# Kernel optimization log

Hardware: AMD Instinct MI355X
Metric: run time of the kernel (lower is better)

The kernel has to match this reference:

```python
import jax, jax.numpy as jnp
import numpy as np

TEMPERATURE = 0.07
NEG = -1e30  # safe stand-in for -inf (keeps grads NaN-free)


def setup_inputs() -> dict:
    key = jax.random.key(0)
    k1, k2 = jax.random.split(key)
    semantic_state = jax.random.normal(k1, (8, 1024, 64), dtype=jnp.float32)
    token_ids = jax.random.randint(k2, (8, 1024), 0, 1000)
    return {"semantic_state": semantic_state, "token_ids": token_ids}


def reference(semantic_state, token_ids):
    # semantic_state: [B, T, D], token_ids: [B, T]
    B, T, D = semantic_state.shape
    N = B * T
    x = semantic_state.reshape(N, D)
    tok = token_ids.reshape(N)

    # L2 normalize (F.normalize, eps=1e-12)
    nrm = jnp.sqrt(jnp.sum(x * x, axis=1, keepdims=True))
    z = x / jnp.maximum(nrm, 1e-12)

    # full cosine-similarity matrix [N, N]
    S = z @ z.T

    # pairs: same token id, excluding self (the per-group similarity structure)
    same = tok[:, None] == tok[None, :]
    eye = jnp.eye(N, dtype=bool)
    mask = same & ~eye

    # per-anchor contrastive term: -logsumexp_{j != i, tok_j == tok_i}(-S_ij / T)
    logits = jnp.where(mask, -S / TEMPERATURE, NEG)
    lse = jax.nn.logsumexp(logits, axis=1)

    valid = mask.any(axis=1)  # anchors whose token repeats (count >= 2)
    per_anchor = jnp.where(valid, -lse, 0.0)

    num_pairs = jnp.sum(mask)  # == sum over groups of N_g*(N_g-1)
    loss = jnp.where(
        num_pairs > 0,
        jnp.sum(per_anchor) / jnp.maximum(num_pairs, 1).astype(S.dtype),
        jnp.array(0.0, dtype=S.dtype),
    )
    return loss
```

## Files before the change

kernel.cpp:

```cpp
#include <hip/hip_runtime.h>
#include <math.h>

#define TEMP 0.07f
#define NTOK 1024
#define CAP 64

__global__ __launch_bounds__(256) void prep_kernel(const float* __restrict__ x,
        const int* __restrict__ tok, float* __restrict__ invn,
        int* __restrict__ cursor, int* __restrict__ bucket, int n) {
    const int lane = threadIdx.x & 63;
    const int w = blockIdx.x * 4 + (threadIdx.x >> 6);
    const int sub = lane & 7, mem = lane >> 3;
    const int row = w * 8 + mem;
    if (row >= n) return;
    const float4* xr = (const float4*)&x[row * 64 + sub * 8];
    float4 a = xr[0], b = xr[1];
    float s = a.x * a.x + a.y * a.y + a.z * a.z + a.w * a.w
            + b.x * b.x + b.y * b.y + b.z * b.z + b.w * b.w;
    s += __shfl_xor(s, 1, 64);
    s += __shfl_xor(s, 2, 64);
    s += __shfl_xor(s, 4, 64);
    if (sub == 0) {
        invn[row] = 1.0f / fmaxf(sqrtf(s), 1e-12f);
        int g = tok[row];
        int slot = atomicAdd(&cursor[g], 1);
        if (slot < CAP) bucket[g * CAP + slot] = row;
    }
}

__global__ __launch_bounds__(256) void lse_kernel(const float* __restrict__ x,
        const int* __restrict__ tok, const float* __restrict__ invn,
        const int* __restrict__ cursor, const int* __restrict__ bucket,
        float* __restrict__ per_anchor, int n) {
    const int lane = threadIdx.x & 63;
    const int i = blockIdx.x * 4 + (threadIdx.x >> 6);
    if (i >= n) return;
    const int g = tok[i];
    const int cnt = min(cursor[g], CAP);
    if (cnt < 2) {
        if (lane == 0) per_anchor[i] = 0.0f;
        return;
    }
    const int sub = lane & 7, mem = lane >> 3;
    const float4* zr = (const float4*)&x[i * 64 + sub * 8];
    float4 za = zr[0], zb = zr[1];
    float sc = invn[i] * (1.0f / TEMP);
    za.x *= sc; za.y *= sc; za.z *= sc; za.w *= sc;
    zb.x *= sc; zb.y *= sc; zb.z *= sc; zb.w *= sc;
    const int* bk = &bucket[g * CAP];
    float S = 0.0f;
    for (int m0 = 0; m0 < cnt; m0 += 8) {
        int mm = m0 + mem;
        bool act = (mm < cnt);
        int j = act ? bk[mm] : 0;
        act = act && (j != i);
        const float4* xr = (const float4*)&x[j * 64 + sub * 8];
        float4 a = xr[0], b = xr[1];
        float iv = invn[j];
        float d = za.x * a.x + za.y * a.y + za.z * a.z + za.w * a.w
                + zb.x * b.x + zb.y * b.y + zb.z * b.z + zb.w * b.w;
        d += __shfl_xor(d, 1, 64);
        d += __shfl_xor(d, 2, 64);
        d += __shfl_xor(d, 4, 64);
        float e = act ? __expf(-d * iv) : 0.0f;
        S += (sub == 0) ? e : 0.0f;
    }
    S += __shfl_xor(S, 8, 64);
    S += __shfl_xor(S, 16, 64);
    S += __shfl_xor(S, 32, 64);
    if (lane == 0) per_anchor[i] = -__logf(S);
}

__global__ __launch_bounds__(1024) void finalize_kernel(
        const float* __restrict__ per_anchor, const int* __restrict__ cursor,
        float* __restrict__ out, int n) {
    int t = threadIdx.x;
    double s = 0.0;
    const float4* pa4 = (const float4*)per_anchor;
    int n4 = n >> 2;
    for (int k = t; k < n4; k += 1024) {
        float4 v = pa4[k];
        s += (double)v.x + (double)v.y + (double)v.z + (double)v.w;
    }
    for (int k = (n4 << 2) + t; k < n; k += 1024) s += (double)per_anchor[k];
    long long c = cursor[t];
    long long p = c * (c - 1);
    #pragma unroll
    for (int o = 32; o; o >>= 1) {
        s += __shfl_xor(s, o, 64);
        p += __shfl_xor(p, o, 64);
    }
    __shared__ double    ls[16];
    __shared__ long long lp[16];
    int wid = t >> 6, lane = t & 63;
    if (lane == 0) { ls[wid] = s; lp[wid] = p; }
    __syncthreads();
    if (wid == 0) {
        double fs = (lane < 16) ? ls[lane] : 0.0;
        long long fp = (lane < 16) ? lp[lane] : 0;
        #pragma unroll
        for (int o = 8; o; o >>= 1) {
            fs += __shfl_xor(fs, o, 64);
            fp += __shfl_xor(fp, o, 64);
        }
        if (lane == 0) out[0] = (fp > 0) ? (float)(fs / (double)fp) : 0.0f;
    }
}

extern "C" void kernel_launch(void* const* d_in, const int* in_sizes, int n_in,
                              void* d_out, int out_size, void* d_ws, size_t ws_size,
                              hipStream_t stream) {
    const float* x = (const float*)d_in[0];
    const int* tok = (const int*)d_in[1];
    int n = in_sizes[1];

    char* ws = (char*)d_ws;
    size_t o = 0;
    int* cursor = (int*)(ws + o);         o += NTOK * 4;
    float* invn = (float*)(ws + o);       o += ((size_t)n * 4 + 255) & ~255UL;
    int* bucket = (int*)(ws + o);         o += (size_t)NTOK * CAP * 4;
    float* per_anchor = (float*)(ws + o);

    hipMemsetAsync(cursor, 0, NTOK * 4, stream);
    prep_kernel<<<(n + 31) / 32, 256, 0, stream>>>(x, tok, invn, cursor, bucket, n);
    lse_kernel<<<(n + 3) / 4, 256, 0, stream>>>(x, tok, invn, cursor, bucket,
                                                per_anchor, n);
    finalize_kernel<<<1, NTOK, 0, stream>>>(per_anchor, cursor, (float*)d_out, n);
}
```

Before: 21.71 us.

## Bucket tokens with shared-memory atomics in one block and recompute norms inline

Replaces the memset plus multi-block prep kernel with a single 1024-thread block that counts and buckets token ids using LDS atomics, then writes the cursors out. Row norms are no longer precomputed into a workspace array; the LSE kernel recomputes each anchor's and each partner's squared norm alongside the dot product, sharing the same shuffle reduction. This drops one launch and the memset, and removes the invn buffer and its global atomics. In exchange, all bucketing is serialized onto one CU and each pair does extra FMAs and a sqrt/reciprocal.

```diff
diff --git a/kernel.cpp b/kernel.cpp
--- a/kernel.cpp
+++ b/kernel.cpp
@@ -5,33 +5,34 @@
 #define NTOK 1024
 #define CAP 64
 
-__global__ __launch_bounds__(256) void prep_kernel(const float* __restrict__ x,
-        const int* __restrict__ tok, float* __restrict__ invn,
+__global__ __launch_bounds__(1024) void bucket_kernel(const int* __restrict__ tok,
         int* __restrict__ cursor, int* __restrict__ bucket, int n) {
-    const int lane = threadIdx.x & 63;
-    const int w = blockIdx.x * 4 + (threadIdx.x >> 6);
-    const int sub = lane & 7, mem = lane >> 3;
-    const int row = w * 8 + mem;
-    if (row >= n) return;
-    const float4* xr = (const float4*)&x[row * 64 + sub * 8];
-    float4 a = xr[0], b = xr[1];
-    float s = a.x * a.x + a.y * a.y + a.z * a.z + a.w * a.w
-            + b.x * b.x + b.y * b.y + b.z * b.z + b.w * b.w;
-    s += __shfl_xor(s, 1, 64);
-    s += __shfl_xor(s, 2, 64);
-    s += __shfl_xor(s, 4, 64);
-    if (sub == 0) {
-        invn[row] = 1.0f / fmaxf(sqrtf(s), 1e-12f);
-        int g = tok[row];
-        int slot = atomicAdd(&cursor[g], 1);
-        if (slot < CAP) bucket[g * CAP + slot] = row;
+    __shared__ int cur[NTOK];
+    int t = threadIdx.x;
+    cur[t] = 0;
+    __syncthreads();
+    const int4* tok4 = (const int4*)tok;
+    int n4 = n >> 2;
+    for (int k = t; k < n4; k += 1024) {
+        int4 v = tok4[k];
+        int base = k << 2;
+        int s0 = atomicAdd(&cur[v.x], 1); if (s0 < CAP) bucket[v.x * CAP + s0] = base;
+        int s1 = atomicAdd(&cur[v.y], 1); if (s1 < CAP) bucket[v.y * CAP + s1] = base + 1;
+        int s2 = atomicAdd(&cur[v.z], 1); if (s2 < CAP) bucket[v.z * CAP + s2] = base + 2;
+        int s3 = atomicAdd(&cur[v.w], 1); if (s3 < CAP) bucket[v.w * CAP + s3] = base + 3;
     }
+    for (int i = (n4 << 2) + t; i < n; i += 1024) {
+        int g = tok[i];
+        int s = atomicAdd(&cur[g], 1);
+        if (s < CAP) bucket[g * CAP + s] = i;
+    }
+    __syncthreads();
+    cursor[t] = cur[t];
 }
 
 __global__ __launch_bounds__(256) void lse_kernel(const float* __restrict__ x,
-        const int* __restrict__ tok, const float* __restrict__ invn,
-        const int* __restrict__ cursor, const int* __restrict__ bucket,
-        float* __restrict__ per_anchor, int n) {
+        const int* __restrict__ tok, const int* __restrict__ cursor,
+        const int* __restrict__ bucket, float* __restrict__ per_anchor, int n) {
     const int lane = threadIdx.x & 63;
     const int i = blockIdx.x * 4 + (threadIdx.x >> 6);
     if (i >= n) return;
@@ -44,7 +45,12 @@
     const int sub = lane & 7, mem = lane >> 3;
     const float4* zr = (const float4*)&x[i * 64 + sub * 8];
     float4 za = zr[0], zb = zr[1];
-    float sc = invn[i] * (1.0f / TEMP);
+    float qi = za.x * za.x + za.y * za.y + za.z * za.z + za.w * za.w
+             + zb.x * zb.x + zb.y * zb.y + zb.z * zb.z + zb.w * zb.w;
+    qi += __shfl_xor(qi, 1, 64);
+    qi += __shfl_xor(qi, 2, 64);
+    qi += __shfl_xor(qi, 4, 64);
+    float sc = (1.0f / TEMP) / fmaxf(sqrtf(qi), 1e-12f);
     za.x *= sc; za.y *= sc; za.z *= sc; za.w *= sc;
     zb.x *= sc; zb.y *= sc; zb.z *= sc; zb.w *= sc;
     const int* bk = &bucket[g * CAP];
@@ -56,12 +62,14 @@
         act = act && (j != i);
         const float4* xr = (const float4*)&x[j * 64 + sub * 8];
         float4 a = xr[0], b = xr[1];
-        float iv = invn[j];
         float d = za.x * a.x + za.y * a.y + za.z * a.z + za.w * a.w
                 + zb.x * b.x + zb.y * b.y + zb.z * b.z + zb.w * b.w;
-        d += __shfl_xor(d, 1, 64);
-        d += __shfl_xor(d, 2, 64);
-        d += __shfl_xor(d, 4, 64);
+        float q = a.x * a.x + a.y * a.y + a.z * a.z + a.w * a.w
+                + b.x * b.x + b.y * b.y + b.z * b.z + b.w * b.w;
+        d += __shfl_xor(d, 1, 64); q += __shfl_xor(q, 1, 64);
+        d += __shfl_xor(d, 2, 64); q += __shfl_xor(q, 2, 64);
+        d += __shfl_xor(d, 4, 64); q += __shfl_xor(q, 4, 64);
+        float iv = 1.0f / fmaxf(sqrtf(q), 1e-12f);
         float e = act ? __expf(-d * iv) : 0.0f;
         S += (sub == 0) ? e : 0.0f;
     }
@@ -117,13 +125,11 @@
     char* ws = (char*)d_ws;
     size_t o = 0;
     int* cursor = (int*)(ws + o);         o += NTOK * 4;
-    float* invn = (float*)(ws + o);       o += ((size_t)n * 4 + 255) & ~255UL;
     int* bucket = (int*)(ws + o);         o += (size_t)NTOK * CAP * 4;
     float* per_anchor = (float*)(ws + o);
 
-    hipMemsetAsync(cursor, 0, NTOK * 4, stream);
-    prep_kernel<<<(n + 31) / 32, 256, 0, stream>>>(x, tok, invn, cursor, bucket, n);
-    lse_kernel<<<(n + 3) / 4, 256, 0, stream>>>(x, tok, invn, cursor, bucket,
+    bucket_kernel<<<1, 1024, 0, stream>>>(tok, cursor, bucket, n);
+    lse_kernel<<<(n + 3) / 4, 256, 0, stream>>>(x, tok, cursor, bucket,
                                                 per_anchor, n);
     finalize_kernel<<<1, NTOK, 0, stream>>>(per_anchor, cursor, (float*)d_out, n);
 }
```

New measurement: 19.02 us. 12.4% less time.
